# Performance work log

Hardware: AMD Instinct MI355X
Metric: run time of the kernel (lower is better)

The kernel has to match this reference:

```python
import jax, jax.numpy as jnp
import numpy as np

A, B, I, J, K = 8, 256, 256, 256, 256  # a=batch, b=tokens, i=s-channels, j=c-channels, k=out_dim


def setup_inputs() -> dict:
    key = jax.random.key(0)
    k1, k2, k3 = jax.random.split(key, 3)
    input_s = jax.random.normal(k1, (A, B, I), dtype=jnp.float32)
    input_c = jax.random.normal(k2, (B, J), dtype=jnp.float32)
    # learned params: w ~ N(0, 0.02), b zeros (as in build())
    w = jax.random.normal(k3, (I, J, K), dtype=jnp.float32) * 0.02
    b = jnp.zeros((K,), dtype=jnp.float32)
    return {"input_s": input_s, "input_c": input_c, "w": w, "b": b}


def reference(input_s, input_c, w, b):
    # Original: tmp = einsum('abi,ijk->abjk', input_s, w); out = einsum('bj,abjk->abk', input_c, tmp) + b
    # Mathematically identical fused bilinear contraction (avoids the [a,b,j,k] intermediate):
    out = jnp.einsum('abi,bj,ijk->abk', input_s, input_c, w)
    return out + b
```

## Files before the change

### kernel.cpp

```cpp
#include <hip/hip_runtime.h>
#include <hip/hip_bf16.h>

#define A_ 8
#define B_ 256
#define I_ 256
#define J_ 256
#define K_ 256

typedef __attribute__((ext_vector_type(8))) short short8_t;
typedef __attribute__((ext_vector_type(4))) float f32x4_t;

static __device__ __forceinline__ uint pack2bf(float a, float b) {
  float2 f2; f2.x = a; f2.y = b;
  __hip_bfloat162 h2 = __float22bfloat162_rn(f2);
  uint r;
  __builtin_memcpy(&r, &h2, 4);
  return r;
}

static __device__ __forceinline__ ushort f2bf(float f) {
  __hip_bfloat16 h = __float2bfloat16(f);
  ushort us;
  __builtin_memcpy(&us, &h, 2);
  return us;
}

static __device__ __forceinline__ float bf2f(ushort h) {
  uint u = ((uint)h) << 16;
  float f;
  __builtin_memcpy(&f, &u, 4);
  return f;
}

#define BM 128
#define BN 128
#define BK 32
#define LDA 40
#define LDB 130

__global__ __launch_bounds__(256, 2) void pass1_kernel(
    const float* __restrict__ cmat, const float* __restrict__ w,
    ushort* __restrict__ u) {
  const int i  = blockIdx.x;
  const int b0 = blockIdx.y * BM;
  const int k0 = blockIdx.z * BN;
  const int tid  = threadIdx.x;
  const int lane = tid & 63;
  const int wave = tid >> 6;
  const int wr = wave >> 1;
  const int wc = wave & 1;

  __shared__ ushort As[BM][LDA];
  __shared__ ushort Bs[BK][LDB];

  const float* wi = w + (size_t)i * (J_ * K_);

  f32x4_t acc[4][4];
#pragma unroll
  for (int m = 0; m < 4; m++)
#pragma unroll
    for (int n = 0; n < 4; n++) acc[m][n] = (f32x4_t)(0.0f);

  const int ar  = tid >> 1;
  const int ajg = (tid & 1) * 16;
  const int bjj = tid >> 3;
  const int bkk = (tid & 7) * 16;

  for (int j0 = 0; j0 < J_; j0 += BK) {
    {
      const float* src = &cmat[(size_t)(b0 + ar) * J_ + j0 + ajg];
      float v[16];
#pragma unroll
      for (int q = 0; q < 4; q++) {
        f32x4_t t4 = *reinterpret_cast<const f32x4_t*>(src + q * 4);
        v[q * 4 + 0] = t4[0]; v[q * 4 + 1] = t4[1];
        v[q * 4 + 2] = t4[2]; v[q * 4 + 3] = t4[3];
      }
      uint* dst = reinterpret_cast<uint*>(&As[ar][ajg]);
#pragma unroll
      for (int q = 0; q < 8; q++) dst[q] = pack2bf(v[2 * q], v[2 * q + 1]);
    }
    {
      const float* src = &wi[(size_t)(j0 + bjj) * K_ + k0 + bkk];
      float v[16];
#pragma unroll
      for (int q = 0; q < 4; q++) {
        f32x4_t t4 = *reinterpret_cast<const f32x4_t*>(src + q * 4);
        v[q * 4 + 0] = t4[0]; v[q * 4 + 1] = t4[1];
        v[q * 4 + 2] = t4[2]; v[q * 4 + 3] = t4[3];
      }
      uint* dst = reinterpret_cast<uint*>(&Bs[bjj][bkk]);
#pragma unroll
      for (int q = 0; q < 8; q++) dst[q] = pack2bf(v[2 * q], v[2 * q + 1]);
    }
    __syncthreads();

    short8_t af[4], bfrag[4];
#pragma unroll
    for (int m = 0; m < 4; m++) {
      const int row = wr * 64 + m * 16 + (lane & 15);
      af[m] = *reinterpret_cast<const short8_t*>(&As[row][(lane >> 4) * 8]);
    }
#pragma unroll
    for (int n = 0; n < 4; n++) {
      const int col = wc * 64 + n * 16 + (lane & 15);
      const int jb  = (lane >> 4) * 8;
      short8_t t;
#pragma unroll
      for (int e = 0; e < 8; e++) t[e] = (short)Bs[jb + e][col];
      bfrag[n] = t;
    }
#pragma unroll
    for (int m = 0; m < 4; m++)
#pragma unroll
      for (int n = 0; n < 4; n++)
        acc[m][n] = __builtin_amdgcn_mfma_f32_16x16x32_bf16(af[m], bfrag[n],
                                                            acc[m][n], 0, 0, 0);
    __syncthreads();
  }

#pragma unroll
  for (int m = 0; m < 4; m++) {
#pragma unroll
    for (int n = 0; n < 4; n++) {
      const int kcol = k0 + wc * 64 + n * 16 + (lane & 15);
#pragma unroll
      for (int r = 0; r < 4; r++) {
        const int brow = b0 + wr * 64 + m * 16 + (lane >> 4) * 4 + r;
        u[((size_t)brow * I_ + i) * K_ + kcol] = f2bf(acc[m][n][r]);
      }
    }
  }
}

__global__ __launch_bounds__(256) void pass2_kernel(
    const float* __restrict__ s, const ushort* __restrict__ u,
    const float* __restrict__ bias, float* __restrict__ out) {
  const int b   = blockIdx.x;
  const int tid = threadIdx.x;
  __shared__ float s_l[A_][I_];
  for (int idx = tid; idx < A_ * I_; idx += 256) {
    const int a = idx >> 8;
    const int i = idx & 255;
    s_l[a][i] = s[(size_t)a * (B_ * I_) + (size_t)b * I_ + i];
  }
  __syncthreads();

  const int k = tid;
  float acc[A_];
#pragma unroll
  for (int a = 0; a < A_; a++) acc[a] = 0.0f;

  const ushort* ub = u + (size_t)b * (I_ * K_) + k;
  for (int i = 0; i < I_; i += 8) {
    float uv[8];
#pragma unroll
    for (int q = 0; q < 8; q++) uv[q] = bf2f(ub[(size_t)(i + q) * K_]);
#pragma unroll
    for (int a = 0; a < A_; a++) {
      const f32x4_t s0 = *reinterpret_cast<const f32x4_t*>(&s_l[a][i]);
      const f32x4_t s1 = *reinterpret_cast<const f32x4_t*>(&s_l[a][i + 4]);
      acc[a] += s0[0] * uv[0] + s0[1] * uv[1] + s0[2] * uv[2] + s0[3] * uv[3] +
                s1[0] * uv[4] + s1[1] * uv[5] + s1[2] * uv[6] + s1[3] * uv[7];
    }
  }

  const float bk = bias[k];
#pragma unroll
  for (int a = 0; a < A_; a++)
    out[((size_t)a * B_ + b) * K_ + k] = acc[a] + bk;
}

__global__ __launch_bounds__(256) void fallback_kernel(
    const float* __restrict__ s, const float* __restrict__ cmat,
    const float* __restrict__ w, const float* __restrict__ bias,
    float* __restrict__ out) {
  const int b = blockIdx.x;
  const int k = threadIdx.x;
  __shared__ float c_l[J_];
  __shared__ float s_l[A_][I_];
  for (int idx = threadIdx.x; idx < J_; idx += 256) c_l[idx] = cmat[(size_t)b * J_ + idx];
  for (int idx = threadIdx.x; idx < A_ * I_; idx += 256) {
    const int a = idx >> 8;
    const int i = idx & 255;
    s_l[a][i] = s[(size_t)a * (B_ * I_) + (size_t)b * I_ + i];
  }
  __syncthreads();
  float acc[A_];
#pragma unroll
  for (int a = 0; a < A_; a++) acc[a] = 0.0f;
  for (int i = 0; i < I_; i++) {
    const float* wrow = w + (size_t)i * (J_ * K_) + k;
    float inner = 0.0f;
    for (int j = 0; j < J_; j++) inner += c_l[j] * wrow[(size_t)j * K_];
#pragma unroll
    for (int a = 0; a < A_; a++) acc[a] += s_l[a][i] * inner;
  }
#pragma unroll
  for (int a = 0; a < A_; a++)
    out[((size_t)a * B_ + b) * K_ + k] = acc[a] + bias[k];
}

extern "C" void kernel_launch(void* const* d_in, const int* in_sizes, int n_in,
                              void* d_out, int out_size, void* d_ws, size_t ws_size,
                              hipStream_t stream) {
  const float* s    = (const float*)d_in[0];
  const float* cmat = (const float*)d_in[1];
  const float* w    = (const float*)d_in[2];
  const float* bias = (const float*)d_in[3];
  float* out = (float*)d_out;

  const size_t need = (size_t)B_ * I_ * K_ * sizeof(ushort);
  if (ws_size >= need) {
    ushort* u = (ushort*)d_ws;
    pass1_kernel<<<dim3(I_, B_ / BM, K_ / BN), dim3(256), 0, stream>>>(cmat, w, u);
    pass2_kernel<<<dim3(B_), dim3(256), 0, stream>>>(s, u, bias, out);
  } else {
    fallback_kernel<<<dim3(B_), dim3(256), 0, stream>>>(s, cmat, w, bias, out);
  }
}
```

Baseline: 48.18 us.

## Restructure bilinear GEMM passes: bf16 pre-cast, full-tile double-buffered pass1, split-i pass2

```diff
diff --git a/kernel.cpp b/kernel.cpp
--- a/kernel.cpp
+++ b/kernel.cpp
@@ -9,6 +9,7 @@
 
 typedef __attribute__((ext_vector_type(8))) short short8_t;
 typedef __attribute__((ext_vector_type(4))) float f32x4_t;
+typedef __attribute__((ext_vector_type(4))) uint u32x4_t;
 
 static __device__ __forceinline__ uint pack2bf(float a, float b) {
   float2 f2; f2.x = a; f2.y = b;
@@ -32,103 +33,107 @@
   return f;
 }
 
-#define BM 128
-#define BN 128
+__global__ __launch_bounds__(256) void prepass_kernel(
+    const float* __restrict__ c, ushort* __restrict__ cbf) {
+  const int idx = blockIdx.x * 256 + threadIdx.x;
+  const f32x4_t v = *reinterpret_cast<const f32x4_t*>(c + (size_t)idx * 4);
+  uint2 r;
+  r.x = pack2bf(v[0], v[1]);
+  r.y = pack2bf(v[2], v[3]);
+  *reinterpret_cast<uint2*>(cbf + (size_t)idx * 4) = r;
+}
+
 #define BK 32
-#define LDA 40
-#define LDB 130
-
-__global__ __launch_bounds__(256, 2) void pass1_kernel(
-    const float* __restrict__ cmat, const float* __restrict__ w,
+#define LDH 40
+
+__global__ __launch_bounds__(512, 2) void pass1_kernel(
+    const ushort* __restrict__ cbf, const float* __restrict__ w,
     ushort* __restrict__ u) {
-  const int i  = blockIdx.x;
-  const int b0 = blockIdx.y * BM;
-  const int k0 = blockIdx.z * BN;
+  const int i    = blockIdx.x;
   const int tid  = threadIdx.x;
   const int lane = tid & 63;
   const int wave = tid >> 6;
-  const int wr = wave >> 1;
-  const int wc = wave & 1;
-
-  __shared__ ushort As[BM][LDA];
-  __shared__ ushort Bs[BK][LDB];
+  const int wr   = wave >> 2;
+  const int wc   = wave & 3;
+  const int lrow = lane & 15;
+  const int lhi  = lane >> 4;
+
+  __shared__ ushort As[2][256][LDH];
+  __shared__ ushort Bt[2][256][LDH];
 
   const float* wi = w + (size_t)i * (J_ * K_);
 
-  f32x4_t acc[4][4];
-#pragma unroll
-  for (int m = 0; m < 4; m++)
+  f32x4_t acc[8][4];
+#pragma unroll
+  for (int m = 0; m < 8; m++)
 #pragma unroll
     for (int n = 0; n < 4; n++) acc[m][n] = (f32x4_t)(0.0f);
 
-  const int ar  = tid >> 1;
-  const int ajg = (tid & 1) * 16;
-  const int bjj = tid >> 3;
-  const int bkk = (tid & 7) * 16;
-
-  for (int j0 = 0; j0 < J_; j0 += BK) {
-    {
-      const float* src = &cmat[(size_t)(b0 + ar) * J_ + j0 + ajg];
-      float v[16];
-#pragma unroll
-      for (int q = 0; q < 4; q++) {
-        f32x4_t t4 = *reinterpret_cast<const f32x4_t*>(src + q * 4);
-        v[q * 4 + 0] = t4[0]; v[q * 4 + 1] = t4[1];
-        v[q * 4 + 2] = t4[2]; v[q * 4 + 3] = t4[3];
-      }
-      uint* dst = reinterpret_cast<uint*>(&As[ar][ajg]);
-#pragma unroll
-      for (int q = 0; q < 8; q++) dst[q] = pack2bf(v[2 * q], v[2 * q + 1]);
-    }
-    {
-      const float* src = &wi[(size_t)(j0 + bjj) * K_ + k0 + bkk];
-      float v[16];
-#pragma unroll
-      for (int q = 0; q < 4; q++) {
-        f32x4_t t4 = *reinterpret_cast<const f32x4_t*>(src + q * 4);
-        v[q * 4 + 0] = t4[0]; v[q * 4 + 1] = t4[1];
-        v[q * 4 + 2] = t4[2]; v[q * 4 + 3] = t4[3];
-      }
-      uint* dst = reinterpret_cast<uint*>(&Bs[bjj][bkk]);
-#pragma unroll
-      for (int q = 0; q < 8; q++) dst[q] = pack2bf(v[2 * q], v[2 * q + 1]);
-    }
+  const int ar = tid >> 1;
+  const int aj = (tid & 1) * 16;
+  const int bk = tid & 255;
+  const int bj = (tid >> 8) * 16;
+
+  short8_t a8[2];
+  float brg[16];
+
+  auto LOAD = [&](int j0) {
+    const ushort* sa = cbf + (size_t)ar * J_ + j0 + aj;
+    a8[0] = *reinterpret_cast<const short8_t*>(sa);
+    a8[1] = *reinterpret_cast<const short8_t*>(sa + 8);
+    const float* sb = wi + (size_t)(j0 + bj) * K_ + bk;
+#pragma unroll
+    for (int q = 0; q < 16; q++) brg[q] = sb[(size_t)q * K_];
+  };
+
+  auto STORE = [&](int buf) {
+    *reinterpret_cast<short8_t*>(&As[buf][ar][aj])     = a8[0];
+    *reinterpret_cast<short8_t*>(&As[buf][ar][aj + 8]) = a8[1];
+    u32x4_t t0, t1;
+#pragma unroll
+    for (int q = 0; q < 4; q++) t0[q] = pack2bf(brg[2 * q], brg[2 * q + 1]);
+#pragma unroll
+    for (int q = 0; q < 4; q++) t1[q] = pack2bf(brg[8 + 2 * q], brg[9 + 2 * q]);
+    *reinterpret_cast<u32x4_t*>(&Bt[buf][bk][bj])     = t0;
+    *reinterpret_cast<u32x4_t*>(&Bt[buf][bk][bj + 8]) = t1;
+  };
+
+  LOAD(0);
+  STORE(0);
+  __syncthreads();
+
+  for (int t = 0; t < 8; ++t) {
+    if (t < 7) LOAD((t + 1) * BK);
+    const int buf = t & 1;
+    short8_t afr[8], bfr[4];
+#pragma unroll
+    for (int m = 0; m < 8; m++)
+      afr[m] = *reinterpret_cast<const short8_t*>(
+          &As[buf][wr * 128 + m * 16 + lrow][lhi * 8]);
+#pragma unroll
+    for (int n = 0; n < 4; n++)
+      bfr[n] = *reinterpret_cast<const short8_t*>(
+          &Bt[buf][wc * 64 + n * 16 + lrow][lhi * 8]);
+#pragma unroll
+    for (int m = 0; m < 8; m++)
+#pragma unroll
+      for (int n = 0; n < 4; n++)
+        acc[m][n] = __builtin_amdgcn_mfma_f32_16x16x32_bf16(afr[m], bfr[n],
+                                                            acc[m][n], 0, 0, 0);
+    if (t < 7) STORE(buf ^ 1);
     __syncthreads();
-
-    short8_t af[4], bfrag[4];
-#pragma unroll
-    for (int m = 0; m < 4; m++) {
-      const int row = wr * 64 + m * 16 + (lane & 15);
-      af[m] = *reinterpret_cast<const short8_t*>(&As[row][(lane >> 4) * 8]);
-    }
+  }
+
+#pragma unroll
+  for (int m = 0; m < 8; m++) {
+    const int brow = wr * 128 + m * 16 + lhi * 4;
 #pragma unroll
     for (int n = 0; n < 4; n++) {
-      const int col = wc * 64 + n * 16 + (lane & 15);
-      const int jb  = (lane >> 4) * 8;
-      short8_t t;
-#pragma unroll
-      for (int e = 0; e < 8; e++) t[e] = (short)Bs[jb + e][col];
-      bfrag[n] = t;
-    }
-#pragma unroll
-    for (int m = 0; m < 4; m++)
-#pragma unroll
-      for (int n = 0; n < 4; n++)
-        acc[m][n] = __builtin_amdgcn_mfma_f32_16x16x32_bf16(af[m], bfrag[n],
-                                                            acc[m][n], 0, 0, 0);
-    __syncthreads();
-  }
-
-#pragma unroll
-  for (int m = 0; m < 4; m++) {
-#pragma unroll
-    for (int n = 0; n < 4; n++) {
-      const int kcol = k0 + wc * 64 + n * 16 + (lane & 15);
-#pragma unroll
-      for (int r = 0; r < 4; r++) {
-        const int brow = b0 + wr * 64 + m * 16 + (lane >> 4) * 4 + r;
-        u[((size_t)brow * I_ + i) * K_ + kcol] = f2bf(acc[m][n][r]);
-      }
+      const int kc = wc * 64 + n * 16 + lrow;
+      ushort* up = u + ((size_t)brow * I_ + i) * K_ + kc;
+#pragma unroll
+      for (int r = 0; r < 4; r++)
+        up[(size_t)r * (I_ * K_)] = f2bf(acc[m][n][r]);
     }
   }
 }
@@ -137,38 +142,60 @@
     const float* __restrict__ s, const ushort* __restrict__ u,
     const float* __restrict__ bias, float* __restrict__ out) {
   const int b   = blockIdx.x;
+  const int a0  = blockIdx.y * 4;
   const int tid = threadIdx.x;
-  __shared__ float s_l[A_][I_];
-  for (int idx = tid; idx < A_ * I_; idx += 256) {
-    const int a = idx >> 8;
-    const int i = idx & 255;
-    s_l[a][i] = s[(size_t)a * (B_ * I_) + (size_t)b * I_ + i];
-  }
-  __syncthreads();
-
-  const int k = tid;
-  float acc[A_];
-#pragma unroll
-  for (int a = 0; a < A_; a++) acc[a] = 0.0f;
-
-  const ushort* ub = u + (size_t)b * (I_ * K_) + k;
-  for (int i = 0; i < I_; i += 8) {
-    float uv[8];
-#pragma unroll
-    for (int q = 0; q < 8; q++) uv[q] = bf2f(ub[(size_t)(i + q) * K_]);
-#pragma unroll
-    for (int a = 0; a < A_; a++) {
-      const f32x4_t s0 = *reinterpret_cast<const f32x4_t*>(&s_l[a][i]);
-      const f32x4_t s1 = *reinterpret_cast<const f32x4_t*>(&s_l[a][i + 4]);
-      acc[a] += s0[0] * uv[0] + s0[1] * uv[1] + s0[2] * uv[2] + s0[3] * uv[3] +
-                s1[0] * uv[4] + s1[1] * uv[5] + s1[2] * uv[6] + s1[3] * uv[7];
+  __shared__ float s_l[4][I_];
+  __shared__ float red[8][4][K_];
+
+#pragma unroll
+  for (int v = 0; v < 4; v++) {
+    const int idx = tid + v * 256;
+    const int a = idx >> 8, ii = idx & 255;
+    s_l[a][ii] = s[((size_t)(a0 + a) * B_ + b) * I_ + ii];
+  }
+  __syncthreads();
+
+  const int kb = (tid & 31) * 8;
+  const int ig = tid >> 5;
+  float acc[4][8];
+#pragma unroll
+  for (int a = 0; a < 4; a++)
+#pragma unroll
+    for (int q = 0; q < 8; q++) acc[a][q] = 0.0f;
+
+  const ushort* ub = u + ((size_t)b * I_ + ig * 32) * K_ + kb;
+  for (int ii = 0; ii < 32; ++ii) {
+    const short8_t uv = *reinterpret_cast<const short8_t*>(ub + (size_t)ii * K_);
+    float f[8];
+#pragma unroll
+    for (int q = 0; q < 8; q++) f[q] = bf2f((ushort)uv[q]);
+    const int i = ig * 32 + ii;
+#pragma unroll
+    for (int a = 0; a < 4; a++) {
+      const float sa = s_l[a][i];
+#pragma unroll
+      for (int q = 0; q < 8; q++) acc[a][q] += sa * f[q];
     }
   }
 
-  const float bk = bias[k];
-#pragma unroll
-  for (int a = 0; a < A_; a++)
-    out[((size_t)a * B_ + b) * K_ + k] = acc[a] + bk;
+#pragma unroll
+  for (int a = 0; a < 4; a++) {
+    f32x4_t r0, r1;
+#pragma unroll
+    for (int q = 0; q < 4; q++) { r0[q] = acc[a][q]; r1[q] = acc[a][4 + q]; }
+    *reinterpret_cast<f32x4_t*>(&red[ig][a][kb])     = r0;
+    *reinterpret_cast<f32x4_t*>(&red[ig][a][kb + 4]) = r1;
+  }
+  __syncthreads();
+
+#pragma unroll
+  for (int v = 0; v < 4; v++) {
+    const int k = tid;
+    float sum = 0.0f;
+#pragma unroll
+    for (int g = 0; g < 8; g++) sum += red[g][v][k];
+    out[((size_t)(a0 + v) * B_ + b) * K_ + k] = sum + bias[k];
+  }
 }
 
 __global__ __launch_bounds__(256) void fallback_kernel(
@@ -210,11 +237,14 @@
   const float* bias = (const float*)d_in[3];
   float* out = (float*)d_out;
 
-  const size_t need = (size_t)B_ * I_ * K_ * sizeof(ushort);
+  const size_t u_elems = (size_t)B_ * I_ * K_;
+  const size_t need = u_elems * sizeof(ushort) + (size_t)B_ * J_ * sizeof(ushort);
   if (ws_size >= need) {
-    ushort* u = (ushort*)d_ws;
-    pass1_kernel<<<dim3(I_, B_ / BM, K_ / BN), dim3(256), 0, stream>>>(cmat, w, u);
-    pass2_kernel<<<dim3(B_), dim3(256), 0, stream>>>(s, u, bias, out);
+    ushort* u   = (ushort*)d_ws;
+    ushort* cbf = (ushort*)d_ws + u_elems;
+    prepass_kernel<<<dim3((B_ * J_) / (256 * 4)), dim3(256), 0, stream>>>(cmat, cbf);
+    pass1_kernel<<<dim3(I_), dim3(512), 0, stream>>>(cbf, w, u);
+    pass2_kernel<<<dim3(B_, 2), dim3(256), 0, stream>>>(s, u, bias, out);
   } else {
     fallback_kernel<<<dim3(B_), dim3(256), 0, stream>>>(s, cmat, w, bias, out);
   }
```

After: 46.10 us. 4.3% less time.
